# Optimization experiments

Measured on AMD Instinct MI355X. Metric: run time of the kernel, lower is better.

Reference implementation:

```python
import jax, jax.numpy as jnp
import numpy as np

# Qwen3-Next-like dims
B, S, HID = 2, 2048, 2048
H, KV, D, ROT = 16, 2, 128, 32
G = H // KV              # kv repeat groups
SCALE = D ** -0.5
EPS = 1e-6
BETA_BIAS, BIAS_CAP = 1.0, 3.0   # L1 logit bias
BETA_POST = 0.5                  # L2 post-softmax rescale
ALPHA_K, ALPHA_V = 0.1, 0.1      # L4 k/v rescale
GMIN, GMAX = 0.9, 1.1
EMIN, EMAX = 0.9, 1.1


def setup_inputs() -> dict:
    key = jax.random.key(0)
    ks = jax.random.split(key, 10)
    hidden_states = jax.random.normal(ks[0], (B, S, HID), jnp.float32)
    # partial rotary embeddings (rot_dim = head_dim // 4)
    pos = jnp.arange(S, dtype=jnp.float32)
    inv = 1.0 / (10000.0 ** (jnp.arange(0, ROT, 2, dtype=jnp.float32) / ROT))
    freqs = pos[:, None] * inv[None, :]
    emb = jnp.concatenate([freqs, freqs], axis=-1)          # [S, ROT]
    cos = jnp.broadcast_to(jnp.cos(emb)[None], (B, S, ROT)).astype(jnp.float32)
    sin = jnp.broadcast_to(jnp.sin(emb)[None], (B, S, ROT)).astype(jnp.float32)
    # additive causal mask [B,1,S,S]
    causal = jnp.tril(jnp.ones((S, S), jnp.bool_))
    attention_mask = jnp.where(causal, 0.0, -1e9).astype(jnp.float32)
    attention_mask = jnp.broadcast_to(attention_mask[None, None], (B, 1, S, S))
    # key prior: positive, sums to 1 over kv_len
    prior = jax.nn.softmax(jax.random.normal(ks[1], (S,), jnp.float32))
    s = 0.02
    Wq = jax.random.normal(ks[2], (HID, H * D * 2), jnp.float32) * s
    Wk = jax.random.normal(ks[3], (HID, KV * D), jnp.float32) * s
    Wv = jax.random.normal(ks[4], (HID, KV * D), jnp.float32) * s
    Wo = jax.random.normal(ks[5], (H * D, HID), jnp.float32) * s
    q_norm_w = 1.0 + 0.02 * jax.random.normal(ks[6], (D,), jnp.float32)
    k_norm_w = 1.0 + 0.02 * jax.random.normal(ks[7], (D,), jnp.float32)
    return {"hidden_states": hidden_states, "cos": cos, "sin": sin,
            "attention_mask": attention_mask, "prior": prior,
            "Wq": Wq, "Wk": Wk, "Wv": Wv, "Wo": Wo,
            "q_norm_w": q_norm_w, "k_norm_w": k_norm_w}


def _rms(x, w):
    return x * jax.lax.rsqrt(jnp.mean(x * x, axis=-1, keepdims=True) + EPS) * w


def _rot_half(x):
    x1, x2 = jnp.split(x, 2, axis=-1)
    return jnp.concatenate([-x2, x1], axis=-1)


def _rope(x, cos, sin):
    # x: [B,h,S,D]; rotary on first ROT dims only (Qwen3-Next partial rotary)
    xr, xp = x[..., :ROT], x[..., ROT:]
    xr = xr * cos + _rot_half(xr) * sin
    return jnp.concatenate([xr, xp], axis=-1)


def reference(hidden_states, cos, sin, attention_mask, prior, Wq, Wk, Wv, Wo, q_norm_w, k_norm_w):
    h = hidden_states
    # gated q projection: chunk into query + gate
    qg = (h @ Wq).reshape(B, S, H, 2 * D)
    q, gate = qg[..., :D], qg[..., D:]
    gate = gate.reshape(B, S, H * D)
    q = _rms(q, q_norm_w).transpose(0, 2, 1, 3)                       # [B,H,S,D]
    k = _rms((h @ Wk).reshape(B, S, KV, D), k_norm_w).transpose(0, 2, 1, 3)  # [B,KV,S,D]
    v = (h @ Wv).reshape(B, S, KV, D).transpose(0, 2, 1, 3)
    c, s_ = cos[:, None], sin[:, None]                                # [B,1,S,ROT]
    q, k = _rope(q, c, s_), _rope(k, c, s_)
    k = jnp.repeat(k, G, axis=1)                                      # GQA expand -> [B,H,S,D]
    v = jnp.repeat(v, G, axis=1)
    # L4: prior-based elementwise k/v rescale with clamped gamma/eta
    pc = prior * S                                                    # mean ~1 over keys
    gamma = jnp.clip(1.0 + ALPHA_K * (pc - 1.0), GMIN, GMAX)
    eta = jnp.clip(1.0 + ALPHA_V * (pc - 1.0), EMIN, EMAX)
    k = k * gamma[None, None, :, None]
    v = v * eta[None, None, :, None]
    scores = jnp.einsum('bhqd,bhkd->bhqk', q, k) * SCALE
    # L1: capped steering bias on logits
    scores = scores + jnp.clip(BETA_BIAS * prior, -BIAS_CAP, BIAS_CAP)[None, None, None, :]
    scores = scores + attention_mask
    probs = jax.nn.softmax(scores.astype(jnp.float32), axis=-1)       # fp32 softmax
    # L2: post-softmax prior rescale + renorm
    p2 = probs * (1.0 + BETA_POST * pc)[None, None, None, :]
    probs = p2 / jnp.sum(p2, axis=-1, keepdims=True)
    out = jnp.einsum('bhqk,bhkd->bhqd', probs.astype(h.dtype), v)
    out = out.transpose(0, 2, 1, 3).reshape(B, S, H * D)
    out = out * jax.nn.sigmoid(gate)                                  # gated attention output
    return out @ Wo
```

## Files before the change

kernel.cpp:

```cpp
#include <hip/hip_runtime.h>
#include <hip/hip_bf16.h>
#include <stdint.h>

#define B_    2
#define S_    2048
#define HID_  2048
#define H_    16
#define KV_   2
#define D_    128
#define ROT_  32
#define QGS   4608
#define SCALE_ 0.08838834764831845f

typedef __attribute__((ext_vector_type(8))) short  short8;
typedef __attribute__((ext_vector_type(4))) float  floatx4;

__device__ __forceinline__ float b2f(unsigned short u) {
  union { unsigned int i; float f; } v; v.i = ((unsigned int)u) << 16; return v.f;
}
__device__ __forceinline__ unsigned short f2b(float f) {
  union { float f; unsigned int i; } v; v.f = f;
  return (unsigned short)((v.i + 0x7fffu + ((v.i >> 16) & 1u)) >> 16);
}
__device__ __forceinline__ void gload_lds16(const unsigned short* g, unsigned short* l) {
  __builtin_amdgcn_global_load_lds((const __attribute__((address_space(1))) void*)g,
                                   (__attribute__((address_space(3))) void*)l, 16, 0, 0);
}

__device__ __forceinline__ void transpose_body(const float* __restrict__ in,
                                               unsigned short* __restrict__ out,
                                               int R, int C, int bx, int by, int t) {
  __shared__ unsigned short tile[64][68];
  int tx = t & 15, ty = t >> 4;
  long c0 = (long)bx * 64, r0 = (long)by * 64;
#pragma unroll
  for (int i = 0; i < 4; i++) {
    int row = ty + 16 * i;
    const float* src = in + (r0 + row) * C + c0 + 4 * tx;
    float4 v = *(const float4*)src;
    tile[row][4 * tx + 0] = f2b(v.x);
    tile[row][4 * tx + 1] = f2b(v.y);
    tile[row][4 * tx + 2] = f2b(v.z);
    tile[row][4 * tx + 3] = f2b(v.w);
  }
  __syncthreads();
#pragma unroll
  for (int i = 0; i < 4; i++) {
    int oc = ty + 16 * i;
    ushort4 v;
    v.x = tile[4 * tx + 0][oc];
    v.y = tile[4 * tx + 1][oc];
    v.z = tile[4 * tx + 2][oc];
    v.w = tile[4 * tx + 3][oc];
    *(ushort4*)(out + (c0 + oc) * R + r0 + 4 * tx) = v;
  }
}

__global__ __launch_bounds__(256) void k_preproc(const float* __restrict__ h_f,
                                                 const float* __restrict__ prior,
                                                 const float* __restrict__ Wq,
                                                 const float* __restrict__ Wk,
                                                 const float* __restrict__ Wv,
                                                 const float* __restrict__ Wo,
                                                 unsigned short* __restrict__ hb,
                                                 unsigned short* __restrict__ WqkvT,
                                                 unsigned short* __restrict__ WoT,
                                                 float* __restrict__ ge,
                                                 float* __restrict__ kbias) {
  int bx = blockIdx.x;
  const int t = threadIdx.x;
  if (bx < 8) {
    int i = bx * 256 + t;
    float p  = prior[i];
    float pc = p * (float)S_;
    float g  = 1.0f + 0.1f * (pc - 1.0f);
    g = fminf(fmaxf(g, 0.9f), 1.1f);
    ge[i] = g;
    float cb = fminf(fmaxf(p, -3.0f), 3.0f);
    kbias[i] = cb + logf(1.0f + 0.5f * pc);
    return;
  }
  bx -= 8;
  if (bx < 4096) {
    long i0 = ((long)bx * 256 + t) * 8;
    float4 a = *(const float4*)(h_f + i0);
    float4 b = *(const float4*)(h_f + i0 + 4);
    short8 v;
    v[0] = (short)f2b(a.x); v[1] = (short)f2b(a.y);
    v[2] = (short)f2b(a.z); v[3] = (short)f2b(a.w);
    v[4] = (short)f2b(b.x); v[5] = (short)f2b(b.y);
    v[6] = (short)f2b(b.z); v[7] = (short)f2b(b.w);
    *(short8*)(hb + i0) = v;
    return;
  }
  bx -= 4096;
  if (bx < 2048) { transpose_body(Wq, WqkvT, 2048, 4096, bx & 63, bx >> 6, t); return; }
  bx -= 2048;
  if (bx < 1024) { transpose_body(Wo, WoT, 2048, 2048, bx & 31, bx >> 5, t); return; }
  bx -= 1024;
  if (bx < 128)  { transpose_body(Wk, WqkvT + (size_t)4096 * 2048, 2048, 256, bx & 3, bx >> 2, t); return; }
  bx -= 128;
  transpose_body(Wv, WqkvT + (size_t)4352 * 2048, 2048, 256, bx & 3, bx >> 2, t);
}

template <int OUT32>
__global__ __launch_bounds__(256, 3) void k_gemm_bt(const unsigned short* __restrict__ A,
                                                    const unsigned short* __restrict__ Bt,
                                                    void* __restrict__ Cv,
                                                    int M, int N, int K) {
  __shared__ __align__(16) unsigned short As[3][128 * 32];
  __shared__ __align__(16) unsigned short Bs[3][128 * 32];
  const int t    = threadIdx.x;
  const int lane = t & 63;
  const int wv   = t >> 6;
  const int wm   = wv >> 1, wn = wv & 1;
  const long m0  = (long)blockIdx.y * 128;
  const long n0  = (long)blockIdx.x * 128;
  const int r15  = lane & 15, g4 = lane >> 4;

  const int srow = lane >> 2;
  const int scol = ((lane & 3) ^ ((lane >> 3) & 3)) * 8;
  const unsigned short* sA0 = A  + (m0 + wv * 16 + srow)       * K + scol;
  const unsigned short* sA1 = A  + (m0 + (wv + 4) * 16 + srow) * K + scol;
  const unsigned short* sB0 = Bt + (n0 + wv * 16 + srow)       * K + scol;
  const unsigned short* sB1 = Bt + (n0 + (wv + 4) * 16 + srow) * K + scol;

  floatx4 acc[4][4];
#pragma unroll
  for (int m = 0; m < 4; m++)
#pragma unroll
    for (int n = 0; n < 4; n++) acc[m][n] = (floatx4){0.f, 0.f, 0.f, 0.f};

  const int nk = K >> 5;
#pragma unroll
  for (int kt = 0; kt < 2; kt++) {
    const int ko = kt * 32;
    gload_lds16(sA0 + ko, &As[kt][wv * 512]);
    gload_lds16(sA1 + ko, &As[kt][(wv + 4) * 512]);
    gload_lds16(sB0 + ko, &Bs[kt][wv * 512]);
    gload_lds16(sB1 + ko, &Bs[kt][(wv + 4) * 512]);
  }

  const int fcol = (g4 ^ ((r15 >> 1) & 3)) * 8;
  int cb = 0;
  for (int k = 0; k < nk; ++k) {
    if (k < nk - 1) asm volatile("s_waitcnt vmcnt(4)" ::: "memory");
    else            asm volatile("s_waitcnt vmcnt(0)" ::: "memory");
    __builtin_amdgcn_sched_barrier(0);
    __builtin_amdgcn_s_barrier();
    __builtin_amdgcn_sched_barrier(0);
    if (k + 2 < nk) {
      const int nb = (cb + 2 >= 3) ? cb - 1 : cb + 2;
      const int ko = (k + 2) * 32;
      gload_lds16(sA0 + ko, &As[nb][wv * 512]);
      gload_lds16(sA1 + ko, &As[nb][(wv + 4) * 512]);
      gload_lds16(sB0 + ko, &Bs[nb][wv * 512]);
      gload_lds16(sB1 + ko, &Bs[nb][(wv + 4) * 512]);
    }
    short8 af[4], bf[4];
#pragma unroll
    for (int m = 0; m < 4; m++)
      af[m] = *(const short8*)(&As[cb][(wm * 64 + m * 16 + r15) * 32 + fcol]);
#pragma unroll
    for (int n = 0; n < 4; n++)
      bf[n] = *(const short8*)(&Bs[cb][(wn * 64 + n * 16 + r15) * 32 + fcol]);
#pragma unroll
    for (int m = 0; m < 4; m++)
#pragma unroll
      for (int n = 0; n < 4; n++)
        acc[m][n] = __builtin_amdgcn_mfma_f32_16x16x32_bf16(af[m], bf[n], acc[m][n], 0, 0, 0);
    cb = (cb == 2) ? 0 : cb + 1;
  }

#pragma unroll
  for (int m = 0; m < 4; m++) {
    const long rbase = m0 + wm * 64 + m * 16 + g4 * 4;
#pragma unroll
    for (int n = 0; n < 4; n++) {
      const long cidx = n0 + wn * 64 + n * 16 + r15;
#pragma unroll
      for (int i = 0; i < 4; i++) {
        if (OUT32) ((float*)Cv)[(rbase + i) * N + cidx] = acc[m][n][i];
        else ((unsigned short*)Cv)[(rbase + i) * N + cidx] = f2b(acc[m][n][i]);
      }
    }
  }
}

__global__ __launch_bounds__(256) void k_qkvpost(const unsigned short* __restrict__ qgkv,
                                                 const float* __restrict__ cosb,
                                                 const float* __restrict__ sinb,
                                                 const float* __restrict__ ge,
                                                 const float* __restrict__ knw,
                                                 unsigned short* __restrict__ kF,
                                                 unsigned short* __restrict__ vF) {
  int bxx = blockIdx.x;
  if (bxx < 2048) {
    int wid  = bxx * 4 + ((int)threadIdx.x >> 6);
    int lane = threadIdx.x & 63;
    int kvb  = wid & 1;
    long bs  = wid >> 1;
    int b = (int)(bs >> 11), s = (int)(bs & 2047);
    int d0 = lane * 2;

    const unsigned short* src = qgkv + bs * QGS + 4096 + kvb * 128 + d0;
    float x0 = b2f(src[0]), x1 = b2f(src[1]);
    float ss = x0 * x0 + x1 * x1;
#pragma unroll
    for (int mask = 1; mask < 64; mask <<= 1) ss += __shfl_xor(ss, mask);
    float rstd = rsqrtf(ss * (1.0f / 128.0f) + 1e-6f);
    float w0 = knw[d0], w1 = knw[d0 + 1];
    float xn0 = x0 * rstd * w0, xn1 = x1 * rstd * w1;
    float p0 = __shfl_xor(xn0, 8), p1 = __shfl_xor(xn1, 8);
    float y0 = xn0, y1 = xn1;
    if (lane < 16) {
      float c0 = cosb[bs * ROT_ + d0], c1 = cosb[bs * ROT_ + d0 + 1];
      float s0 = sinb[bs * ROT_ + d0], s1 = sinb[bs * ROT_ + d0 + 1];
      float sgn = (lane < 8) ? -1.0f : 1.0f;
      y0 = xn0 * c0 + sgn * p0 * s0;
      y1 = xn1 * c1 + sgn * p1 * s1;
    }
    float g = ge[s];
    unsigned int pack = (unsigned int)f2b(y0 * g) | ((unsigned int)f2b(y1 * g) << 16);
    size_t off = (size_t)(b * KV_ + kvb) * 262144
               + (size_t)((s >> 4) * 4 + (d0 >> 5)) * 512
               + (size_t)(((s & 15) + (((d0 >> 3) & 3)) * 16)) * 8 + (d0 & 7);
    *(unsigned int*)(kF + off) = pack;
  } else {
    int bx  = bxx - 2048;
    int scn = bx & 7, d = (bx >> 3) & 127, kvb = (bx >> 10) & 1, b = bx >> 11;
    int s = scn * 256 + threadIdx.x;
    float v = b2f(qgkv[((long)(b * S_ + s)) * QGS + 4352 + kvb * 128 + d]);
    v *= ge[s];
    size_t off = (size_t)(b * KV_ + kvb) * 262144
               + (size_t)((s >> 6) * 16 + (d >> 4) * 2 + ((s >> 5) & 1)) * 512
               + (size_t)((d & 15) + ((s >> 3) & 3) * 16) * 8 + (s & 7);
    vF[off] = f2b(v);
  }
}

__global__ __launch_bounds__(256) void k_attn(const unsigned short* __restrict__ qgkv,
                                              const unsigned short* __restrict__ kF,
                                              const unsigned short* __restrict__ vF,
                                              const float* __restrict__ kbias,
                                              const float* __restrict__ cosb,
                                              const float* __restrict__ sinb,
                                              const float* __restrict__ qnw,
                                              unsigned short* __restrict__ ag) {
  __shared__ __align__(16) unsigned short KL[2][8192];
  __shared__ __align__(16) unsigned short Ps[4][16 * 88];
  const int t = threadIdx.x;
  const int lane = t & 63, wv = t >> 6;
  const int r15 = lane & 15, g4 = lane >> 4;
  const int p = blockIdx.x;
  const int xcd = p & 7;
  const int grp = xcd >> 1;
  const int mem = ((p >> 3) << 1) | (xcd & 1);
  const int head = mem & 7;
  const int quad = 31 - (mem >> 3);
  const int b = grp >> 1, kvh = grp & 1;
  const int hh = kvh * 8 + head;
  const int strip = quad * 4 + wv;
  const int q0s = strip * 16;
  const int ntiles = quad + 1;

  const unsigned short* kFg = kF + (size_t)(b * KV_ + kvh) * 262144;
  const unsigned short* vFg = vF + (size_t)(b * KV_ + kvh) * 262144;

  short8 qf[4];
  {
    const int q = q0s + r15;
    const unsigned short* qp = qgkv + ((size_t)(b * S_) + q) * QGS + hh * 256 + g4 * 8;
    float xn[4][8];
    float ssq = 0.f;
#pragma unroll
    for (int kb = 0; kb < 4; kb++) {
      short8 qr = *(const short8*)(qp + kb * 32);
#pragma unroll
      for (int e = 0; e < 8; e++) {
        float x = b2f((unsigned short)qr[e]);
        xn[kb][e] = x;
        ssq += x * x;
      }
    }
    ssq += __shfl_xor(ssq, 16);
    ssq += __shfl_xor(ssq, 32);
    float rstd = rsqrtf(ssq * (1.0f / 128.0f) + 1e-6f);
#pragma unroll
    for (int kb = 0; kb < 4; kb++) {
      float4 w0 = *(const float4*)(&qnw[kb * 32 + g4 * 8]);
      float4 w1 = *(const float4*)(&qnw[kb * 32 + g4 * 8 + 4]);
      xn[kb][0] *= rstd * w0.x; xn[kb][1] *= rstd * w0.y;
      xn[kb][2] *= rstd * w0.z; xn[kb][3] *= rstd * w0.w;
      xn[kb][4] *= rstd * w1.x; xn[kb][5] *= rstd * w1.y;
      xn[kb][6] *= rstd * w1.z; xn[kb][7] *= rstd * w1.w;
    }
    {
      const float* cbp = cosb + ((size_t)(b * S_) + q) * ROT_ + g4 * 8;
      const float* sbp = sinb + ((size_t)(b * S_) + q) * ROT_ + g4 * 8;
      float4 c0 = *(const float4*)(cbp), c1 = *(const float4*)(cbp + 4);
      float4 s0 = *(const float4*)(sbp), s1 = *(const float4*)(sbp + 4);
      float cv[8] = {c0.x, c0.y, c0.z, c0.w, c1.x, c1.y, c1.z, c1.w};
      float sv[8] = {s0.x, s0.y, s0.z, s0.w, s1.x, s1.y, s1.z, s1.w};
      float sgn = (g4 < 2) ? -1.0f : 1.0f;
#pragma unroll
      for (int e = 0; e < 8; e++) {
        float part = __shfl_xor(xn[0][e], 32);
        xn[0][e] = xn[0][e] * cv[e] + sgn * part * sv[e];
      }
    }
#pragma unroll
    for (int kb = 0; kb < 4; kb++)
#pragma unroll
      for (int e = 0; e < 8; e++) qf[kb][e] = (short)f2b(xn[kb][e]);
  }

  floatx4 oacc[8];
#pragma unroll
  for (int nd = 0; nd < 8; nd++) oacc[nd] = (floatx4){0.f, 0.f, 0.f, 0.f};
  float mrow = -1e30f, lrw = 0.f;

#pragma unroll
  for (int i = 0; i < 4; i++)
    gload_lds16(kFg + (size_t)wv * 2048 + i * 512 + lane * 8, &KL[0][wv * 2048 + i * 512]);
  __syncthreads();

  int cur = 0;
  for (int tile = 0; tile < ntiles; tile++) {
    if (tile + 1 < ntiles) {
      const size_t src = (size_t)(tile + 1) * 8192 + wv * 2048 + lane * 8;
#pragma unroll
      for (int i = 0; i < 4; i++)
        gload_lds16(kFg + src + i * 512, &KL[cur ^ 1][wv * 2048 + i * 512]);
    }

    floatx4 sacc[4];
#pragma unroll
    for (int n = 0; n < 4; n++) sacc[n] = (floatx4){0.f, 0.f, 0.f, 0.f};
    __builtin_amdgcn_s_setprio(1);
#pragma unroll
    for (int n = 0; n < 4; n++) {
      const unsigned short* kl = &KL[cur][n * 2048 + lane * 8];
      short8 a0 = *(const short8*)(kl);
      short8 a1 = *(const short8*)(kl + 512);
      short8 a2 = *(const short8*)(kl + 1024);
      short8 a3 = *(const short8*)(kl + 1536);
      sacc[n] = __builtin_amdgcn_mfma_f32_16x16x32_bf16(a0, qf[0], sacc[n], 0, 0, 0);
      sacc[n] = __builtin_amdgcn_mfma_f32_16x16x32_bf16(a1, qf[1], sacc[n], 0, 0, 0);
      sacc[n] = __builtin_amdgcn_mfma_f32_16x16x32_bf16(a2, qf[2], sacc[n], 0, 0, 0);
      sacc[n] = __builtin_amdgcn_mfma_f32_16x16x32_bf16(a3, qf[3], sacc[n], 0, 0, 0);
    }
    __builtin_amdgcn_s_setprio(0);

    const unsigned short* vt = vFg + (size_t)tile * 8192 + lane * 8;
    short8 vfA[8];
#pragma unroll
    for (int nd = 0; nd < 8; nd++) vfA[nd] = *(const short8*)(vt + (nd * 2) * 512);

    const bool last = (tile == ntiles - 1);
    float scf[4][4];
#pragma unroll
    for (int n = 0; n < 4; n++) {
      const int j0 = tile * 64;
      float4 kb4 = *(const float4*)(&kbias[j0 + n * 16 + g4 * 4]);
#pragma unroll
      for (int i = 0; i < 4; i++) {
        float kbv = (i == 0) ? kb4.x : (i == 1) ? kb4.y : (i == 2) ? kb4.z : kb4.w;
        float v = sacc[n][i] * SCALE_ + kbv;
        if (last) {
          int jg = j0 + n * 16 + g4 * 4 + i;
          if (jg > q0s + r15) v = -1e30f;
        }
        scf[n][i] = v;
      }
    }
    float pmax = scf[0][0];
#pragma unroll
    for (int n = 0; n < 4; n++)
#pragma unroll
      for (int i = 0; i < 4; i++) pmax = fmaxf(pmax, scf[n][i]);
    pmax = fmaxf(pmax, __shfl_xor(pmax, 16));
    pmax = fmaxf(pmax, __shfl_xor(pmax, 32));
    if (__any(pmax > mrow + 8.0f)) {
      float mn = fmaxf(mrow, pmax);
      float aq = __expf(mrow - mn);
      mrow = mn;
      lrw *= aq;
      float ai[4];
#pragma unroll
      for (int i = 0; i < 4; i++) ai[i] = __shfl(aq, g4 * 4 + i);
#pragma unroll
      for (int nd = 0; nd < 8; nd++)
#pragma unroll
        for (int i = 0; i < 4; i++) oacc[nd][i] *= ai[i];
    }
    float rsum = 0.f;
#pragma unroll
    for (int n = 0; n < 4; n++)
#pragma unroll
      for (int i = 0; i < 4; i++) {
        float pv = __expf(scf[n][i] - mrow);
        scf[n][i] = pv;
        rsum += pv;
      }
    rsum += __shfl_xor(rsum, 16);
    rsum += __shfl_xor(rsum, 32);
    lrw += rsum;

#pragma unroll
    for (int n = 0; n < 4; n++) {
      unsigned int lo = (unsigned int)f2b(scf[n][0]) | ((unsigned int)f2b(scf[n][1]) << 16);
      unsigned int hi = (unsigned int)f2b(scf[n][2]) | ((unsigned int)f2b(scf[n][3]) << 16);
      uint2 w; w.x = lo; w.y = hi;
      *(uint2*)(&Ps[wv][r15 * 88 + n * 16 + g4 * 4]) = w;
    }

    short8 vfB[8];
#pragma unroll
    for (int nd = 0; nd < 8; nd++) vfB[nd] = *(const short8*)(vt + (nd * 2 + 1) * 512);

    {
      __builtin_amdgcn_s_setprio(1);
      short8 pa0 = *(const short8*)(&Ps[wv][r15 * 88 + g4 * 8]);
#pragma unroll
      for (int nd = 0; nd < 8; nd++)
        oacc[nd] = __builtin_amdgcn_mfma_f32_16x16x32_bf16(pa0, vfA[nd], oacc[nd], 0, 0, 0);
      short8 pa1 = *(const short8*)(&Ps[wv][r15 * 88 + 32 + g4 * 8]);
#pragma unroll
      for (int nd = 0; nd < 8; nd++)
        oacc[nd] = __builtin_amdgcn_mfma_f32_16x16x32_bf16(pa1, vfB[nd], oacc[nd], 0, 0, 0);
      __builtin_amdgcn_s_setprio(0);
    }
    __syncthreads();
    cur ^= 1;
  }

  float il[4];
#pragma unroll
  for (int i = 0; i < 4; i++) il[i] = __shfl(lrw, g4 * 4 + i);
#pragma unroll
  for (int i = 0; i < 4; i++) {
    int q = q0s + g4 * 4 + i;
    float inv = 1.0f / il[i];
    const unsigned short* gptr = qgkv + ((size_t)(b * S_ + q)) * QGS + hh * 256 + 128;
    unsigned short* aptr = ag + ((size_t)(b * S_ + q)) * (H_ * D_) + hh * D_;
#pragma unroll
    for (int nd = 0; nd < 8; nd++) {
      int d = nd * 16 + r15;
      float gt = b2f(gptr[d]);
      float sg = 1.0f / (1.0f + __expf(-gt));
      aptr[d] = f2b(oacc[nd][i] * inv * sg);
    }
  }
}

extern "C" void kernel_launch(void* const* d_in, const int* in_sizes, int n_in,
                              void* d_out, int out_size, void* d_ws, size_t ws_size,
                              hipStream_t stream) {
  const float* h_f   = (const float*)d_in[0];
  const float* cosb  = (const float*)d_in[1];
  const float* sinb  = (const float*)d_in[2];
  const float* prior = (const float*)d_in[4];
  const float* Wq    = (const float*)d_in[5];
  const float* Wk    = (const float*)d_in[6];
  const float* Wv    = (const float*)d_in[7];
  const float* Wo    = (const float*)d_in[8];
  const float* qnw   = (const float*)d_in[9];
  const float* knw   = (const float*)d_in[10];

  char* ws = (char*)d_ws;
  size_t off = 0;
  auto alloc = [&](size_t bytes) { char* p = ws + off; off += (bytes + 255) & ~(size_t)255; return p; };
  unsigned short* hb    = (unsigned short*)alloc((size_t)4096 * 2048 * 2);
  unsigned short* WqkvT = (unsigned short*)alloc((size_t)4608 * 2048 * 2);
  unsigned short* WoT   = (unsigned short*)alloc((size_t)2048 * 2048 * 2);
  unsigned short* qgkv  = (unsigned short*)alloc((size_t)4096 * QGS * 2);
  unsigned short* kF    = (unsigned short*)alloc((size_t)B_ * KV_ * S_ * D_ * 2);
  unsigned short* vF    = (unsigned short*)alloc((size_t)B_ * KV_ * S_ * D_ * 2);
  float* ge    = (float*)alloc((size_t)S_ * 4);
  float* kbias = (float*)alloc((size_t)S_ * 4);
  unsigned short* ag = hb;

  dim3 blk(256);
  k_preproc<<<dim3(7432), blk, 0, stream>>>(h_f, prior, Wq, Wk, Wv, Wo,
                                            hb, WqkvT, WoT, ge, kbias);
  k_gemm_bt<0><<<dim3(36, 32), blk, 0, stream>>>(hb, WqkvT, qgkv, 4096, QGS, 2048);
  k_qkvpost<<<dim3(6144), blk, 0, stream>>>(qgkv, cosb, sinb, ge, knw, kF, vF);
  k_attn<<<dim3(1024), blk, 0, stream>>>(qgkv, kF, vF, kbias, cosb, sinb, qnw, ag);
  k_gemm_bt<1><<<dim3(16, 32), blk, 0, stream>>>(ag, WoT, d_out, 4096, 2048, 2048);
}
```

Baseline: 261.5 us.

## Store hidden states in MFMA-fragment layout and load A operand directly to registers

The bf16 conversion of hidden states now writes a fragment-tiled layout in which each 16x32 k-chunk is laid out contiguously in MFMA operand order. A new QKV GEMM kernel reads A fragments straight from global memory into registers, double-buffered across k-steps, and stages only B through LDS. This removes the A-side LDS traffic and halves shared memory per block, in exchange for more register pressure and direct global loads on the critical path. The output GEMM keeps the old kernel and reuses the buffer for row-major attention output.

```diff
diff --git a/kernel.cpp b/kernel.cpp
--- a/kernel.cpp
+++ b/kernel.cpp
@@ -62,7 +62,7 @@
                                                  const float* __restrict__ Wk,
                                                  const float* __restrict__ Wv,
                                                  const float* __restrict__ Wo,
-                                                 unsigned short* __restrict__ hb,
+                                                 unsigned short* __restrict__ hbF,
                                                  unsigned short* __restrict__ WqkvT,
                                                  unsigned short* __restrict__ WoT,
                                                  float* __restrict__ ge,
@@ -90,7 +90,11 @@
     v[2] = (short)f2b(a.z); v[3] = (short)f2b(a.w);
     v[4] = (short)f2b(b.x); v[5] = (short)f2b(b.y);
     v[6] = (short)f2b(b.z); v[7] = (short)f2b(b.w);
-    *(short8*)(hb + i0) = v;
+    int row = (int)(i0 >> 11);
+    int k   = (int)(i0 & 2047);
+    size_t dst = ((size_t)((row >> 4) * 64 + (k >> 5))) * 512
+               + (size_t)((row & 15) + ((k >> 3) & 3) * 16) * 8;
+    *(short8*)(hbF + dst) = v;
     return;
   }
   bx -= 4096;
@@ -101,6 +105,120 @@
   if (bx < 128)  { transpose_body(Wk, WqkvT + (size_t)4096 * 2048, 2048, 256, bx & 3, bx >> 2, t); return; }
   bx -= 128;
   transpose_body(Wv, WqkvT + (size_t)4352 * 2048, 2048, 256, bx & 3, bx >> 2, t);
+}
+
+template <int OUT32>
+__global__ __launch_bounds__(256) void k_gemm_af(const unsigned short* __restrict__ hbF,
+                                                 const unsigned short* __restrict__ Bt,
+                                                 void* __restrict__ Cv,
+                                                 int M, int N, int K) {
+  __shared__ __align__(16) unsigned short Bs[3][128 * 32];
+  const int t    = threadIdx.x;
+  const int lane = t & 63;
+  const int wv   = t >> 6;
+  const int wm   = wv >> 1, wn = wv & 1;
+  const long m0  = (long)blockIdx.y * 128;
+  const long n0  = (long)blockIdx.x * 128;
+  const int r15  = lane & 15, g4 = lane >> 4;
+
+  const int srow = lane >> 2;
+  const int scol = ((lane & 3) ^ ((lane >> 3) & 3)) * 8;
+  const unsigned short* sB0 = Bt + (n0 + wv * 16 + srow)       * K + scol;
+  const unsigned short* sB1 = Bt + (n0 + (wv + 4) * 16 + srow) * K + scol;
+
+  const int KC = K >> 5;
+  const unsigned short* aBase = hbF + ((size_t)(((m0 >> 4) + wm * 4) * KC)) * 512 + lane * 8;
+
+  floatx4 acc[4][4];
+#pragma unroll
+  for (int m = 0; m < 4; m++)
+#pragma unroll
+    for (int n = 0; n < 4; n++) acc[m][n] = (floatx4){0.f, 0.f, 0.f, 0.f};
+
+  const int nk = K >> 5;
+  gload_lds16(sB0,      &Bs[0][wv * 512]);
+  gload_lds16(sB1,      &Bs[0][(wv + 4) * 512]);
+  gload_lds16(sB0 + 32, &Bs[1][wv * 512]);
+  gload_lds16(sB1 + 32, &Bs[1][(wv + 4) * 512]);
+  short8 afA[4], afB[4];
+#pragma unroll
+  for (int m = 0; m < 4; m++) afA[m] = *(const short8*)(aBase + (size_t)(m * KC) * 512);
+#pragma unroll
+  for (int m = 0; m < 4; m++) afB[m] = *(const short8*)(aBase + (size_t)(m * KC + 1) * 512);
+
+  const int fcol = (g4 ^ ((r15 >> 1) & 3)) * 8;
+  int cb = 0;
+  for (int k2 = 0; k2 < nk; k2 += 2) {
+    {
+      const int k = k2;
+      asm volatile("s_waitcnt vmcnt(10)" ::: "memory");
+      __builtin_amdgcn_sched_barrier(0);
+      __builtin_amdgcn_s_barrier();
+      __builtin_amdgcn_sched_barrier(0);
+      if (k + 2 < nk) {
+        const int nb = (cb + 2 >= 3) ? cb - 1 : cb + 2;
+        gload_lds16(sB0 + (k + 2) * 32, &Bs[nb][wv * 512]);
+        gload_lds16(sB1 + (k + 2) * 32, &Bs[nb][(wv + 4) * 512]);
+      }
+      short8 bf[4];
+#pragma unroll
+      for (int n = 0; n < 4; n++)
+        bf[n] = *(const short8*)(&Bs[cb][(wn * 64 + n * 16 + r15) * 32 + fcol]);
+#pragma unroll
+      for (int m = 0; m < 4; m++)
+#pragma unroll
+        for (int n = 0; n < 4; n++)
+          acc[m][n] = __builtin_amdgcn_mfma_f32_16x16x32_bf16(afA[m], bf[n], acc[m][n], 0, 0, 0);
+      if (k + 2 < nk) {
+#pragma unroll
+        for (int m = 0; m < 4; m++)
+          afA[m] = *(const short8*)(aBase + (size_t)(m * KC + k + 2) * 512);
+      }
+      cb = (cb == 2) ? 0 : cb + 1;
+    }
+    {
+      const int k = k2 + 1;
+      if (k2 + 2 >= nk) asm volatile("s_waitcnt vmcnt(4)" ::: "memory");
+      else              asm volatile("s_waitcnt vmcnt(10)" ::: "memory");
+      __builtin_amdgcn_sched_barrier(0);
+      __builtin_amdgcn_s_barrier();
+      __builtin_amdgcn_sched_barrier(0);
+      if (k + 2 < nk) {
+        const int nb = (cb + 2 >= 3) ? cb - 1 : cb + 2;
+        gload_lds16(sB0 + (k + 2) * 32, &Bs[nb][wv * 512]);
+        gload_lds16(sB1 + (k + 2) * 32, &Bs[nb][(wv + 4) * 512]);
+      }
+      short8 bf[4];
+#pragma unroll
+      for (int n = 0; n < 4; n++)
+        bf[n] = *(const short8*)(&Bs[cb][(wn * 64 + n * 16 + r15) * 32 + fcol]);
+#pragma unroll
+      for (int m = 0; m < 4; m++)
+#pragma unroll
+        for (int n = 0; n < 4; n++)
+          acc[m][n] = __builtin_amdgcn_mfma_f32_16x16x32_bf16(afB[m], bf[n], acc[m][n], 0, 0, 0);
+      if (k + 2 < nk) {
+#pragma unroll
+        for (int m = 0; m < 4; m++)
+          afB[m] = *(const short8*)(aBase + (size_t)(m * KC + k + 2) * 512);
+      }
+      cb = (cb == 2) ? 0 : cb + 1;
+    }
+  }
+
+#pragma unroll
+  for (int m = 0; m < 4; m++) {
+    const long rbase = m0 + wm * 64 + m * 16 + g4 * 4;
+#pragma unroll
+    for (int n = 0; n < 4; n++) {
+      const long cidx = n0 + wn * 64 + n * 16 + r15;
+#pragma unroll
+      for (int i = 0; i < 4; i++) {
+        if (OUT32) ((float*)Cv)[(rbase + i) * N + cidx] = acc[m][n][i];
+        else ((unsigned short*)Cv)[(rbase + i) * N + cidx] = f2b(acc[m][n][i]);
+      }
+    }
+  }
 }
 
 template <int OUT32>
@@ -471,7 +589,7 @@
   char* ws = (char*)d_ws;
   size_t off = 0;
   auto alloc = [&](size_t bytes) { char* p = ws + off; off += (bytes + 255) & ~(size_t)255; return p; };
-  unsigned short* hb    = (unsigned short*)alloc((size_t)4096 * 2048 * 2);
+  unsigned short* hbF   = (unsigned short*)alloc((size_t)4096 * 2048 * 2);
   unsigned short* WqkvT = (unsigned short*)alloc((size_t)4608 * 2048 * 2);
   unsigned short* WoT   = (unsigned short*)alloc((size_t)2048 * 2048 * 2);
   unsigned short* qgkv  = (unsigned short*)alloc((size_t)4096 * QGS * 2);
@@ -479,12 +597,12 @@
   unsigned short* vF    = (unsigned short*)alloc((size_t)B_ * KV_ * S_ * D_ * 2);
   float* ge    = (float*)alloc((size_t)S_ * 4);
   float* kbias = (float*)alloc((size_t)S_ * 4);
-  unsigned short* ag = hb;
+  unsigned short* ag = hbF;
 
   dim3 blk(256);
   k_preproc<<<dim3(7432), blk, 0, stream>>>(h_f, prior, Wq, Wk, Wv, Wo,
-                                            hb, WqkvT, WoT, ge, kbias);
-  k_gemm_bt<0><<<dim3(36, 32), blk, 0, stream>>>(hb, WqkvT, qgkv, 4096, QGS, 2048);
+                                            hbF, WqkvT, WoT, ge, kbias);
+  k_gemm_af<0><<<dim3(36, 32), blk, 0, stream>>>(hbF, WqkvT, qgkv, 4096, QGS, 2048);
   k_qkvpost<<<dim3(6144), blk, 0, stream>>>(qgkv, cosb, sinb, ge, knw, kF, vF);
   k_attn<<<dim3(1024), blk, 0, stream>>>(qgkv, kF, vF, kbias, cosb, sinb, qnw, ag);
   k_gemm_bt<1><<<dim3(16, 32), blk, 0, stream>>>(ag, WoT, d_out, 4096, 2048, 2048);
```

After: 261.3 us. Within noise of the previous version (-0.0%).
